# Kernel optimization log

Hardware: AMD Instinct MI355X
Metric: run time of the kernel (lower is better)

The kernel has to match this reference:

```python
import jax, jax.numpy as jnp
import numpy as np
import math

IN_F = 512
OUT_F = 512
N_EXPERTS = 8
N_GROUPS = 32
TOKENS_PER_GROUP = 2048
N_TOKENS = N_GROUPS * TOKENS_PER_GROUP


def setup_inputs() -> dict:
    key = jax.random.key(0)
    ks = jax.random.split(key, 6)
    k = math.sqrt(1.0 / IN_F)  # init scale from reset_parameters
    x = jax.random.normal(ks[0], (N_TOKENS, IN_F), dtype=jnp.float32)
    # routing coefficients per group (e.g. softmax-like positive weights)
    coefficients = jax.random.uniform(ks[1], (N_GROUPS, N_EXPERTS), dtype=jnp.float32)
    coefficients = coefficients / coefficients.sum(axis=1, keepdims=True)
    weight_experts = jax.random.uniform(ks[2], (N_EXPERTS, OUT_F, IN_F), minval=-k, maxval=k, dtype=jnp.float32)
    bias_experts = jax.random.uniform(ks[3], (N_EXPERTS, OUT_F), minval=-k, maxval=k, dtype=jnp.float32)
    weight_shared = jax.random.uniform(ks[4], (OUT_F, IN_F), minval=-k, maxval=k, dtype=jnp.float32)
    bias_shared = jax.random.uniform(ks[5], (OUT_F,), minval=-k, maxval=k, dtype=jnp.float32)
    sizes = jnp.full((N_GROUPS,), TOKENS_PER_GROUP, dtype=jnp.int32)
    return {
        "x": x,
        "coefficients": coefficients,
        "weight_experts": weight_experts,
        "bias_experts": bias_experts,
        "weight_shared": weight_shared,
        "bias_shared": bias_shared,
        "sizes": sizes,
    }


def reference(x, coefficients, weight_experts, bias_experts, weight_shared, bias_shared, sizes):
    # Routed path: per-group mixed weights  W_g = sum_e coeff[g,e] * W_e  (+ shared)
    G = coefficients.shape[0]
    N = x.shape[0]
    T = N // G  # equal group sizes (static), equivalent to torch.split(x, sizes)
    mixed_w = jnp.einsum('ge,eoi->goi', coefficients, weight_experts) + weight_shared[None]
    mixed_b = jnp.einsum('ge,eo->go', coefficients, bias_experts) + bias_shared[None]
    xg = x.reshape(G, T, -1)                      # [G, T, in]
    out = jnp.einsum('gti,goi->gto', xg, mixed_w) # grouped GEMM, F.linear per group
    out = out + mixed_b[:, None, :]
    return out.reshape(N, -1)
```

## Files before the change

kernel.cpp:

```cpp
#include <hip/hip_runtime.h>
#include <stdint.h>

typedef unsigned short u16;
typedef __attribute__((ext_vector_type(8))) __bf16 bf16x8;
typedef __attribute__((ext_vector_type(4))) __bf16 bf16x4;
typedef __attribute__((ext_vector_type(4))) float f32x4;

#define NGROUPS 32
#define TOK 2048
#define IN_F 512
#define OUT_F 512
#define NEXP 8
#define BM 128
#define BN 128
#define BK 64
#define NKT (IN_F / BK)

__device__ __forceinline__ u16 f2bf(float f) {
    unsigned int u = __float_as_uint(f);
    unsigned int r = (u + 0x7fffu + ((u >> 16) & 1u)) >> 16;
    return (u16)r;
}

__global__ __launch_bounds__(256) void mix_w_kernel(
    const float* __restrict__ coeff, const float* __restrict__ We,
    const float* __restrict__ Wsh, u16* __restrict__ mw)
{
    __shared__ float cs[NGROUPS * NEXP];
    int tid = threadIdx.x;
    cs[tid] = coeff[tid];
    __syncthreads();

    size_t idx = ((size_t)blockIdx.x * 256 + tid) * 4;
    f32x4 wsh = *(const f32x4*)(Wsh + idx);
    f32x4 we[NEXP];
#pragma unroll
    for (int e = 0; e < NEXP; ++e)
        we[e] = *(const f32x4*)(We + (size_t)e * OUT_F * IN_F + idx);

    int g0 = blockIdx.y * 8;
    for (int g = g0; g < g0 + 8; ++g) {
        f32x4 a = wsh;
#pragma unroll
        for (int e = 0; e < NEXP; ++e) {
            float c = cs[g * NEXP + e];
            a[0] += c * we[e][0];
            a[1] += c * we[e][1];
            a[2] += c * we[e][2];
            a[3] += c * we[e][3];
        }
        unsigned int ow[2];
        ow[0] = (unsigned int)f2bf(a[0]) | ((unsigned int)f2bf(a[1]) << 16);
        ow[1] = (unsigned int)f2bf(a[2]) | ((unsigned int)f2bf(a[3]) << 16);
        *(uint2*)(mw + (size_t)g * OUT_F * IN_F + idx) = *(const uint2*)ow;
    }
}

__global__ __launch_bounds__(256) void gemm_kernel(
    const float* __restrict__ x, const u16* __restrict__ mw,
    const float* __restrict__ coeff, const float* __restrict__ be,
    const float* __restrict__ bsh, float* __restrict__ out)
{
    __shared__ __align__(16) u16 As[2][BM * BK];
    __shared__ __align__(16) u16 Bs[2][BN * BK];

    int bid = blockIdx.x;
    int xcd = bid & 7;
    int i   = bid >> 3;
    int g = xcd * 4 + (i >> 6);
    int t = i & 63;
    int mtile = t >> 2;
    int ntile = t & 3;

    const float* Ag = x + ((size_t)g * TOK + (size_t)mtile * BM) * IN_F;
    const u16*   Bg = mw + (size_t)g * OUT_F * IN_F + (size_t)ntile * BN * IN_F;

    int tid  = threadIdx.x;
    int lane = tid & 63;
    int wave = tid >> 6;
    int wm = wave >> 1, wn = wave & 1;
    int lm = lane & 15, lq = lane >> 4;

    f32x4 acc[4][4];
#pragma unroll
    for (int mi = 0; mi < 4; ++mi)
#pragma unroll
        for (int ni = 0; ni < 4; ++ni)
            acc[mi][ni] = f32x4{0.f, 0.f, 0.f, 0.f};

    f32x4 areg[8];
#pragma unroll
    for (int q = 0; q < 4; ++q) {
        int r = q * 32 + (tid >> 3);
        int c = (tid & 7) ^ (r & 7);
        __builtin_amdgcn_global_load_lds(
            (const __attribute__((address_space(1))) void*)(Bg + (size_t)r * IN_F + c * 8),
            (__attribute__((address_space(3))) void*)(&Bs[0][((size_t)q * 256 + tid) * 8]),
            16, 0, 0);
    }
#pragma unroll
    for (int j = 0; j < 8; ++j) {
        int L = j * 256 + tid;
        areg[j] = *(const f32x4*)(Ag + (size_t)(L >> 4) * IN_F + (L & 15) * 4);
    }
#pragma unroll
    for (int j = 0; j < 8; ++j) {
        int L = j * 256 + tid;
        int r = L >> 4, c4 = L & 15;
        int p = (c4 >> 1) ^ (r & 7);
        bf16x4 bv;
        bv[0] = (__bf16)areg[j][0];
        bv[1] = (__bf16)areg[j][1];
        bv[2] = (__bf16)areg[j][2];
        bv[3] = (__bf16)areg[j][3];
        *(bf16x4*)(&As[0][r * 64 + p * 8 + (c4 & 1) * 4]) = bv;
    }
    __syncthreads();

#pragma unroll
    for (int kk = 0; kk < NKT; ++kk) {
        const int cur = kk & 1;
        const int nxt = cur ^ 1;
        const int k1 = (kk + 1) * BK;
        const bool more = (kk + 1 < NKT);

        if (more) {
#pragma unroll
            for (int j = 0; j < 8; ++j) {
                int L = j * 256 + tid;
                areg[j] = *(const f32x4*)(Ag + (size_t)(L >> 4) * IN_F + k1 + (L & 15) * 4);
            }
#pragma unroll
            for (int q = 0; q < 4; ++q) {
                int r = q * 32 + (tid >> 3);
                int c = (tid & 7) ^ (r & 7);
                __builtin_amdgcn_global_load_lds(
                    (const __attribute__((address_space(1))) void*)(Bg + (size_t)r * IN_F + k1 + c * 8),
                    (__attribute__((address_space(3))) void*)(&Bs[nxt][((size_t)q * 256 + tid) * 8]),
                    16, 0, 0);
            }
        }

#pragma unroll
        for (int ks = 0; ks < 2; ++ks) {
            bf16x8 af[4], bfv[4];
#pragma unroll
            for (int mi = 0; mi < 4; ++mi) {
                int r = wm * 64 + mi * 16 + lm;
                int p = (ks * 4 + lq) ^ (r & 7);
                af[mi] = *(const bf16x8*)(&As[cur][r * 64 + p * 8]);
            }
#pragma unroll
            for (int ni = 0; ni < 4; ++ni) {
                int r = wn * 64 + ni * 16 + lm;
                int p = (ks * 4 + lq) ^ (r & 7);
                bfv[ni] = *(const bf16x8*)(&Bs[cur][r * 64 + p * 8]);
            }
#pragma unroll
            for (int mi = 0; mi < 4; ++mi)
#pragma unroll
                for (int ni = 0; ni < 4; ++ni)
                    acc[mi][ni] = __builtin_amdgcn_mfma_f32_16x16x32_bf16(
                        af[mi], bfv[ni], acc[mi][ni], 0, 0, 0);
        }

        if (more) {
#pragma unroll
            for (int j = 0; j < 8; ++j) {
                int L = j * 256 + tid;
                int r = L >> 4, c4 = L & 15;
                int p = (c4 >> 1) ^ (r & 7);
                bf16x4 bv;
                bv[0] = (__bf16)areg[j][0];
                bv[1] = (__bf16)areg[j][1];
                bv[2] = (__bf16)areg[j][2];
                bv[3] = (__bf16)areg[j][3];
                *(bf16x4*)(&As[nxt][r * 64 + p * 8 + (c4 & 1) * 4]) = bv;
            }
            __syncthreads();
        }
    }

    int c0 = ntile * BN + wn * 64;
    float cg[NEXP];
#pragma unroll
    for (int e = 0; e < NEXP; ++e) cg[e] = coeff[g * NEXP + e];
    float bias[4];
#pragma unroll
    for (int ni = 0; ni < 4; ++ni) {
        int o = c0 + ni * 16 + lm;
        float v = bsh[o];
#pragma unroll
        for (int e = 0; e < NEXP; ++e) v += cg[e] * be[e * OUT_F + o];
        bias[ni] = v;
    }

    size_t rowbase = (size_t)g * TOK + (size_t)mtile * BM + (size_t)wm * 64;
#pragma unroll
    for (int mi = 0; mi < 4; ++mi) {
#pragma unroll
        for (int rr = 0; rr < 4; ++rr) {
            size_t row = rowbase + mi * 16 + lq * 4 + rr;
            float* orow = out + row * OUT_F;
#pragma unroll
            for (int ni = 0; ni < 4; ++ni)
                orow[c0 + ni * 16 + lm] = acc[mi][ni][rr] + bias[ni];
        }
    }
}

extern "C" void kernel_launch(void* const* d_in, const int* in_sizes, int n_in,
                              void* d_out, int out_size, void* d_ws, size_t ws_size,
                              hipStream_t stream) {
    const float* x     = (const float*)d_in[0];
    const float* coeff = (const float*)d_in[1];
    const float* We    = (const float*)d_in[2];
    const float* be    = (const float*)d_in[3];
    const float* Wsh   = (const float*)d_in[4];
    const float* bsh   = (const float*)d_in[5];
    float* out = (float*)d_out;

    u16* mw = (u16*)d_ws;

    mix_w_kernel<<<dim3(OUT_F * IN_F / (256 * 4), 4), 256, 0, stream>>>(coeff, We, Wsh, mw);

    int grid = NGROUPS * (TOK / BM) * (OUT_F / BN);
    gemm_kernel<<<grid, 256, 0, stream>>>(x, mw, coeff, be, bsh, out);
}
```

Before: 295.8 us.

## Triple-buffer B tiles with two-ahead prefetch and manual vmcnt waits

```diff
diff --git a/kernel.cpp b/kernel.cpp
--- a/kernel.cpp
+++ b/kernel.cpp
@@ -62,7 +62,7 @@
     const float* __restrict__ bsh, float* __restrict__ out)
 {
     __shared__ __align__(16) u16 As[2][BM * BK];
-    __shared__ __align__(16) u16 Bs[2][BN * BK];
+    __shared__ __align__(16) u16 Bs[3][BN * BK];
 
     int bid = blockIdx.x;
     int xcd = bid & 7;
@@ -90,18 +90,21 @@
 
     f32x4 areg[8];
 #pragma unroll
-    for (int q = 0; q < 4; ++q) {
-        int r = q * 32 + (tid >> 3);
-        int c = (tid & 7) ^ (r & 7);
-        __builtin_amdgcn_global_load_lds(
-            (const __attribute__((address_space(1))) void*)(Bg + (size_t)r * IN_F + c * 8),
-            (__attribute__((address_space(3))) void*)(&Bs[0][((size_t)q * 256 + tid) * 8]),
-            16, 0, 0);
-    }
-#pragma unroll
     for (int j = 0; j < 8; ++j) {
         int L = j * 256 + tid;
         areg[j] = *(const f32x4*)(Ag + (size_t)(L >> 4) * IN_F + (L & 15) * 4);
+    }
+#pragma unroll
+    for (int kb = 0; kb < 2; ++kb) {
+#pragma unroll
+        for (int q = 0; q < 4; ++q) {
+            int r = q * 32 + (tid >> 3);
+            int c = (tid & 7) ^ (r & 7);
+            __builtin_amdgcn_global_load_lds(
+                (const __attribute__((address_space(1))) void*)(Bg + (size_t)r * IN_F + kb * BK + c * 8),
+                (__attribute__((address_space(3))) void*)(&Bs[kb][((size_t)q * 256 + tid) * 8]),
+                16, 0, 0);
+        }
     }
 #pragma unroll
     for (int j = 0; j < 8; ++j) {
@@ -115,56 +118,70 @@
         bv[3] = (__bf16)areg[j][3];
         *(bf16x4*)(&As[0][r * 64 + p * 8 + (c4 & 1) * 4]) = bv;
     }
-    __syncthreads();
+    asm volatile("s_waitcnt vmcnt(4)" ::: "memory");
+    __builtin_amdgcn_sched_barrier(0);
+    asm volatile("s_waitcnt lgkmcnt(0)" ::: "memory");
+    __builtin_amdgcn_sched_barrier(0);
+    __builtin_amdgcn_s_barrier();
 
 #pragma unroll
     for (int kk = 0; kk < NKT; ++kk) {
-        const int cur = kk & 1;
-        const int nxt = cur ^ 1;
-        const int k1 = (kk + 1) * BK;
-        const bool more = (kk + 1 < NKT);
-
-        if (more) {
+        const int cur  = kk & 1;
+        const int bcur = kk % 3;
+        const bool moreA = (kk + 1 < NKT);
+        const bool moreB = (kk + 2 < NKT);
+
+        bf16x8 af[2][4], bfv[2][4];
+#pragma unroll
+        for (int ks = 0; ks < 2; ++ks) {
+#pragma unroll
+            for (int mi = 0; mi < 4; ++mi) {
+                int r = wm * 64 + mi * 16 + lm;
+                int p = (ks * 4 + lq) ^ (r & 7);
+                af[ks][mi] = *(const bf16x8*)(&As[cur][r * 64 + p * 8]);
+            }
+#pragma unroll
+            for (int ni = 0; ni < 4; ++ni) {
+                int r = wn * 64 + ni * 16 + lm;
+                int p = (ks * 4 + lq) ^ (r & 7);
+                bfv[ks][ni] = *(const bf16x8*)(&Bs[bcur][r * 64 + p * 8]);
+            }
+        }
+
+        if (moreA) {
+            int k1 = (kk + 1) * BK;
 #pragma unroll
             for (int j = 0; j < 8; ++j) {
                 int L = j * 256 + tid;
                 areg[j] = *(const f32x4*)(Ag + (size_t)(L >> 4) * IN_F + k1 + (L & 15) * 4);
             }
+        }
+        if (moreB) {
+            int k2 = (kk + 2) * BK;
+            const int bnxt2 = (kk + 2) % 3;
 #pragma unroll
             for (int q = 0; q < 4; ++q) {
                 int r = q * 32 + (tid >> 3);
                 int c = (tid & 7) ^ (r & 7);
                 __builtin_amdgcn_global_load_lds(
-                    (const __attribute__((address_space(1))) void*)(Bg + (size_t)r * IN_F + k1 + c * 8),
-                    (__attribute__((address_space(3))) void*)(&Bs[nxt][((size_t)q * 256 + tid) * 8]),
+                    (const __attribute__((address_space(1))) void*)(Bg + (size_t)r * IN_F + k2 + c * 8),
+                    (__attribute__((address_space(3))) void*)(&Bs[bnxt2][((size_t)q * 256 + tid) * 8]),
                     16, 0, 0);
             }
         }
 
-#pragma unroll
-        for (int ks = 0; ks < 2; ++ks) {
-            bf16x8 af[4], bfv[4];
-#pragma unroll
-            for (int mi = 0; mi < 4; ++mi) {
-                int r = wm * 64 + mi * 16 + lm;
-                int p = (ks * 4 + lq) ^ (r & 7);
-                af[mi] = *(const bf16x8*)(&As[cur][r * 64 + p * 8]);
-            }
-#pragma unroll
-            for (int ni = 0; ni < 4; ++ni) {
-                int r = wn * 64 + ni * 16 + lm;
-                int p = (ks * 4 + lq) ^ (r & 7);
-                bfv[ni] = *(const bf16x8*)(&Bs[cur][r * 64 + p * 8]);
-            }
+        __builtin_amdgcn_s_setprio(1);
+#pragma unroll
+        for (int ks = 0; ks < 2; ++ks)
 #pragma unroll
             for (int mi = 0; mi < 4; ++mi)
 #pragma unroll
                 for (int ni = 0; ni < 4; ++ni)
                     acc[mi][ni] = __builtin_amdgcn_mfma_f32_16x16x32_bf16(
-                        af[mi], bfv[ni], acc[mi][ni], 0, 0, 0);
-        }
-
-        if (more) {
+                        af[ks][mi], bfv[ks][ni], acc[mi][ni], 0, 0, 0);
+        __builtin_amdgcn_s_setprio(0);
+
+        if (moreA) {
 #pragma unroll
             for (int j = 0; j < 8; ++j) {
                 int L = j * 256 + tid;
@@ -175,9 +192,18 @@
                 bv[1] = (__bf16)areg[j][1];
                 bv[2] = (__bf16)areg[j][2];
                 bv[3] = (__bf16)areg[j][3];
-                *(bf16x4*)(&As[nxt][r * 64 + p * 8 + (c4 & 1) * 4]) = bv;
-            }
-            __syncthreads();
+                *(bf16x4*)(&As[cur ^ 1][r * 64 + p * 8 + (c4 & 1) * 4]) = bv;
+            }
+
+            if (moreB) {
+                asm volatile("s_waitcnt vmcnt(4)" ::: "memory");
+            } else {
+                asm volatile("s_waitcnt vmcnt(0)" ::: "memory");
+            }
+            __builtin_amdgcn_sched_barrier(0);
+            asm volatile("s_waitcnt lgkmcnt(0)" ::: "memory");
+            __builtin_amdgcn_sched_barrier(0);
+            __builtin_amdgcn_s_barrier();
         }
     }
 
```

After: 283.2 us. 1.04x faster.
